# Kernel optimization log

Hardware: AMD Instinct MI355X
Metric: run time of the kernel (lower is better)

Reference implementation:

```python
import jax, jax.numpy as jnp
import numpy as np

E = 23   # unique_experts_num
K = 3    # act_experts_num
D = 1024 # in_features
H = 768  # hidden_features (0.75 * dim, per MOEBlock mlp_ratio)


def setup_inputs() -> dict:
    key = jax.random.key(0)
    ks = jax.random.split(key, 12)
    s_in = 1.0 / np.sqrt(D)
    s_hid = 1.0 / np.sqrt(H)
    x = jax.random.normal(ks[0], (4, 1024, D), dtype=jnp.float32)
    gate_W = jax.random.normal(ks[1], (D, E), dtype=jnp.float32) * s_in
    gate_b = jnp.zeros((E,), jnp.float32)
    bias = jnp.zeros((E,), jnp.float32)  # registered buffer, init to zeros
    W1 = jax.random.normal(ks[2], (E, D, H), dtype=jnp.float32) * s_in
    b1 = jnp.zeros((E, H), jnp.float32)
    W2 = jax.random.normal(ks[3], (E, H, D), dtype=jnp.float32) * s_hid
    b2 = jnp.zeros((E, D), jnp.float32)
    sW1 = jax.random.normal(ks[4], (D, H), dtype=jnp.float32) * s_in
    sb1 = jnp.zeros((H,), jnp.float32)
    sW2 = jax.random.normal(ks[5], (H, D), dtype=jnp.float32) * s_hid
    sb2 = jnp.zeros((D,), jnp.float32)
    return {"x": x, "gate_W": gate_W, "gate_b": gate_b, "bias": bias,
            "W1": W1, "b1": b1, "W2": W2, "b2": b2,
            "sW1": sW1, "sb1": sb1, "sW2": sW2, "sb2": sb2}


def reference(x, gate_W, gate_b, bias, W1, b1, W2, b2, sW1, sb1, sW2, sb2):
    o_shape = x.shape
    xt = x.reshape(-1, o_shape[-1])          # [T, D]
    T = xt.shape[0]

    # gating: sigmoid gate, top-k indices chosen on (gate + bias), weights gathered from gate
    gate = jax.nn.sigmoid(xt @ gate_W + gate_b)            # [T, E]
    _, top_idx = jax.lax.top_k(gate + bias, K)             # [T, K]
    top_w = jnp.take_along_axis(gate, top_idx, axis=-1)    # [T, K]
    top_w = top_w / jnp.sum(top_w, axis=-1, keepdims=True)

    # combine matrix: C[t, e] = normalized gate weight if e in top-k of token t else 0
    C = jnp.zeros((T, E), xt.dtype).at[jnp.arange(T)[:, None], top_idx].set(top_w)

    # all-expert dense compute (math-equivalent to dispatch/compute/combine)
    h = jax.nn.gelu(jnp.einsum('td,edh->eth', xt, W1) + b1[:, None, :], approximate=False)
    y = jnp.einsum('eth,ehd->etd', h, W2) + b2[:, None, :]  # [E, T, D]
    moe_out = jnp.einsum('etd,te->td', y, C)                # weighted combine

    # shared expert applied to every token
    shared = jax.nn.gelu(xt @ sW1 + sb1, approximate=False) @ sW2 + sb2
    out = shared + moe_out

    # aux load-balance loss
    gate_norm = gate / jnp.sum(gate, axis=-1, keepdims=True)
    P = jnp.mean(gate_norm, axis=0)                          # [E]
    counts = jnp.sum(jax.nn.one_hot(top_idx, E, dtype=jnp.float32), axis=(0, 1))  # [E]
    F = E * counts / (K * T)
    aux_loss = jnp.sum(P * F)

    return out.reshape(o_shape), aux_loss, counts.astype(jnp.int32)
```

## Files before the change

### kernel.cpp

```cpp
#include <hip/hip_runtime.h>
#include <math.h>

#define TT 4096
#define DD 1024
#define HH 768
#define NE 23
#define NG 24
#define BM 128
#define BN 128
#define BK 64
#define MAXT 160
#define KB1 16
#define KB2 12
#define NY1 6
#define NY2 8
#define NWG1 (MAXT*NY1)
#define NWG2 (MAXT*NY2)
#define GATE_BLKS 1024
#define CVT1_BLKS 2304
#define CVT_TOT   4608

#define WS_CURS   0
#define WS_OFFS   576
#define WS_TOTAL  640
#define WS_T2E    672
#define WS_T2A    832
#define WS_TOKE   1024
#define WS_TOKW   13312
#define WS_LTOK   25600
#define WS_LW     41984
#define WS_PPART  58368
#define WS_CPART  81920
#define WS_SIDX   106496
#define XB_OFF  ((size_t)524288)
#define H_OFF   ((size_t)8912896)
#define W1B_OFF ((size_t)34078720)
#define W2B_OFF ((size_t)71827456)

typedef short bf16x8 __attribute__((ext_vector_type(8)));
typedef float f32x4 __attribute__((ext_vector_type(4)));

#define S_BARRIER() asm volatile("s_barrier" ::: "memory")
#define WAIT_VM0()  asm volatile("s_waitcnt vmcnt(0)" ::: "memory")

__device__ inline unsigned short bfr(float f) {
    unsigned u = __float_as_uint(f);
    u += 0x7fffu + ((u >> 16) & 1u);
    return (unsigned short)(u >> 16);
}
__device__ inline unsigned bfr2(float lo, float hi) {
    return (unsigned)bfr(lo) | ((unsigned)bfr(hi) << 16);
}
__device__ inline float b2f(unsigned short u) {
    return __uint_as_float((unsigned)u << 16);
}

__device__ __forceinline__ void gl_lds16(const void* g, void* l) {
    __builtin_amdgcn_global_load_lds(
        (const __attribute__((address_space(1))) unsigned int*)g,
        (__attribute__((address_space(3))) unsigned int*)l, 16, 0, 0);
}

__global__ __launch_bounds__(256) void k_gatecvt(
    const float* __restrict__ x, const float* __restrict__ gW,
    const float* __restrict__ gb, const float* __restrict__ bias,
    const float* __restrict__ W1, const float* __restrict__ sW1,
    const float* __restrict__ W2, const float* __restrict__ sW2,
    int* __restrict__ tokE, float* __restrict__ tokW,
    float* __restrict__ Ppart, int* __restrict__ Cpart,
    unsigned short* __restrict__ xb,
    unsigned short* __restrict__ W1b, unsigned short* __restrict__ W2b)
{
    __shared__ __align__(16) char smem[16896];
    const int tid = threadIdx.x;

    if (blockIdx.x >= GATE_BLKS) {
        int id = blockIdx.x - GATE_BLKS;
        const float* src; unsigned short* dst;
        int N, kb0, n0, KBt, e;
        if (id < CVT1_BLKS) {
            N = HH; KBt = KB1;
            n0 = (id % 12) * 64; kb0 = ((id / 12) % 8) * 2; e = id / 96;
            src = (e < NE) ? (W1 + (size_t)e * DD * HH) : sW1;
            dst = W1b;
        } else {
            id -= CVT1_BLKS;
            N = DD; KBt = KB2;
            n0 = (id % 16) * 64; kb0 = ((id / 16) % 6) * 2; e = id / 96;
            src = (e < NE) ? (W2 + (size_t)e * HH * DD) : sW2;
            dst = W2b;
        }
        unsigned (*Ls)[32][65] = (unsigned (*)[32][65])smem;
        const int c = (tid & 15) * 4, r2l = tid >> 4;
        #pragma unroll
        for (int t = 0; t < 2; t++) {
            const float* tsrc = src + (size_t)(kb0 + t) * 64 * N + n0;
            #pragma unroll
            for (int pass = 0; pass < 2; pass++) {
                int row2 = pass * 16 + r2l;
                float4 v0 = *(const float4*)(tsrc + (size_t)(2 * row2) * N + c);
                float4 v1 = *(const float4*)(tsrc + (size_t)(2 * row2 + 1) * N + c);
                uint4 o;
                o.x = bfr2(v0.x, v1.x); o.y = bfr2(v0.y, v1.y);
                o.z = bfr2(v0.z, v1.z); o.w = bfr2(v0.w, v1.w);
                *(uint4*)&Ls[t][row2][c] = o;
            }
        }
        __syncthreads();
        #pragma unroll
        for (int t = 0; t < 2; t++) {
            unsigned short* dbase = dst + ((size_t)(e * KBt + kb0 + t) * N + n0) * 64;
            #pragma unroll
            for (int half = 0; half < 2; half++) {
                int g = half * 256 + tid;
                int n = g >> 3, p = g & 7;
                int j4 = (p ^ (n & 7)) * 4;
                uint4 o;
                o.x = Ls[t][j4 + 0][n]; o.y = Ls[t][j4 + 1][n];
                o.z = Ls[t][j4 + 2][n]; o.w = Ls[t][j4 + 3][n];
                *(uint4*)(dbase + n * 64 + p * 8) = o;
            }
        }
        return;
    }

    float (*xs)[DD] = (float (*)[DD])smem;
    float (*gv)[NE] = (float (*)[NE])(smem + 16384);
    float* ginvs    = (float*)(smem + 16768);
    int (*sel)[3]   = (int (*)[3])(smem + 16784);
    const int bid = blockIdx.x;
    const int t0 = bid * 4;
    {
        const float4* srcx = (const float4*)(x + (size_t)t0 * DD);
        float4* dstx = (float4*)&xs[0][0];
        #pragma unroll
        for (int i = 0; i < 4; i++) dstx[tid + 256 * i] = srcx[tid + 256 * i];
    }
    __syncthreads();
    {
        const float* xf = &xs[0][0];
        unsigned short* xd = xb + (size_t)t0 * DD;
        #pragma unroll
        for (int it = 0; it < 4; it++) {
            int o = it * 1024 + tid * 4;
            ushort4 u = make_ushort4(bfr(xf[o]), bfr(xf[o + 1]), bfr(xf[o + 2]), bfr(xf[o + 3]));
            *(ushort4*)(xd + o) = u;
        }
    }
    const int w = tid >> 6, l = tid & 63;
    const int t = t0 + w;
    if (l < NE) {
        const float* gc = gW + l;
        const float* xw = xs[w];
        float s[4] = {0.f, 0.f, 0.f, 0.f};
        #pragma unroll 2
        for (int d0 = 0; d0 < DD; d0 += 16) {
            float g[16];
            #pragma unroll
            for (int j = 0; j < 16; j++) g[j] = gc[(d0 + j) * NE];
            #pragma unroll
            for (int j = 0; j < 16; j++) s[j & 3] = fmaf(xw[d0 + j], g[j], s[j & 3]);
        }
        float sv = (s[0] + s[1]) + (s[2] + s[3]) + gb[l];
        gv[w][l] = 1.f / (1.f + expf(-sv));
    }
    __syncthreads();
    if (l == 0) {
        unsigned chosen = 0;
        int be[3]; float bw[3];
        float gsum = 0.f;
        for (int e = 0; e < NE; e++) gsum += gv[w][e];
        #pragma unroll
        for (int k = 0; k < 3; k++) {
            float m = -1e30f; int mi = 0;
            for (int e = 0; e < NE; e++) {
                float kv = gv[w][e] + bias[e];
                if (!((chosen >> e) & 1u) && kv > m) { m = kv; mi = e; }
            }
            chosen |= 1u << mi;
            be[k] = mi; bw[k] = gv[w][mi];
        }
        float inv = 1.f / (bw[0] + bw[1] + bw[2]);
        #pragma unroll
        for (int k = 0; k < 3; k++) {
            tokE[t * 3 + k] = be[k];
            tokW[t * 3 + k] = bw[k] * inv;
            sel[w][k] = be[k];
        }
        ginvs[w] = 1.f / gsum;
    }
    __syncthreads();
    if (tid < NE) {
        float p = gv[0][tid] * ginvs[0] + gv[1][tid] * ginvs[1]
                + gv[2][tid] * ginvs[2] + gv[3][tid] * ginvs[3];
        Ppart[tid * 1024 + bid] = p;
        int c = 0;
        #pragma unroll
        for (int w2 = 0; w2 < 4; w2++)
            #pragma unroll
            for (int k = 0; k < 3; k++) c += (sel[w2][k] == tid);
        Cpart[tid * 1024 + bid] = c;
    }
}

__global__ __launch_bounds__(256) void k_reduce(
    const float* __restrict__ Ppart, const int* __restrict__ Cpart,
    int* __restrict__ counts, float* __restrict__ Psum)
{
    const int e = blockIdx.x;
    const int tid = threadIdx.x;
    float s = 0.f; int c = 0;
    for (int i = tid; i < 1024; i += 256) {
        s += Ppart[e * 1024 + i];
        c += Cpart[e * 1024 + i];
    }
    #pragma unroll
    for (int off = 32; off >= 1; off >>= 1) {
        s += __shfl_down(s, off, 64);
        c += __shfl_down(c, off, 64);
    }
    __shared__ float ss[4]; __shared__ int sc[4];
    if ((tid & 63) == 0) { ss[tid >> 6] = s; sc[tid >> 6] = c; }
    __syncthreads();
    if (tid == 0) {
        Psum[e] = ss[0] + ss[1] + ss[2] + ss[3];
        counts[e] = sc[0] + sc[1] + sc[2] + sc[3];
    }
}

__global__ void k_scan(const int* __restrict__ counts, const float* __restrict__ Psum,
                       int* __restrict__ offs, int* __restrict__ total,
                       int* __restrict__ t2e, int* __restrict__ t2a,
                       int* __restrict__ curs, float* __restrict__ outAux)
{
    const int tid = threadIdx.x;
    for (int i = tid; i < NE * 16; i += 256) curs[i] = 0;
    if (tid != 0) return;
    int off = 0, toff = 0;
    for (int e = 0; e < NG; e++) {
        int c = (e < NE) ? counts[e] : TT;
        offs[e] = off;
        int nt = (c + BM - 1) / BM;
        for (int t = 0; t < nt; t++) {
            t2e[toff + t] = e;
            t2a[toff + t] = off + t * BM;
        }
        off += c; toff += nt;
    }
    offs[NG] = off;
    *total = toff;
    float aux = 0.f;
    for (int e = 0; e < NE; e++) {
        float P = Psum[e] / (float)TT;
        float F = (float)NE * (float)counts[e] / (float)(3 * TT);
        aux += P * F;
    }
    outAux[0] = aux;
    for (int e = 0; e < NE; e++) outAux[1 + e] = (float)counts[e];
}

__global__ void k_scatter(const int* __restrict__ tokE, const float* __restrict__ tokW,
                          const int* __restrict__ offs, int* __restrict__ curs,
                          int* __restrict__ ltok, float* __restrict__ lw,
                          int* __restrict__ sidx)
{
    int t = blockIdx.x * 256 + threadIdx.x;
    if (t >= TT) return;
    #pragma unroll
    for (int k = 0; k < 3; k++) {
        int e = tokE[t * 3 + k];
        int pos = atomicAdd(&curs[e * 16], 1);
        int idx = offs[e] + pos;
        ltok[idx] = t; lw[idx] = tokW[t * 3 + k];
        sidx[t * 3 + k] = idx;
    }
    ltok[3 * TT + t] = t;
    lw[3 * TT + t] = 1.f;
}

__global__ __launch_bounds__(256) void k_mm1(
    const unsigned short* __restrict__ xb, const unsigned short* __restrict__ W1b,
    const float* __restrict__ b1, const float* __restrict__ sb1,
    const int* __restrict__ t2e, const int* __restrict__ t2a,
    const int* __restrict__ offs, const int* __restrict__ total,
    const int* __restrict__ ltok, unsigned short* __restrict__ H)
{
    const int id = blockIdx.x;
    const int wg = (id & 7) * (NWG1 / 8) + (id >> 3);
    const int ns = wg / MAXT;
    const int tb = wg % MAXT;
    if (tb >= *total) return;
    const int e = t2e[tb];
    const int a0 = t2a[tb];
    const int acount = min(offs[e + 1] - a0, BM);
    const float* bb = (e < NE) ? (b1 + e * HH) : sb1;
    const int nb = ns * BN;

    __shared__ unsigned short As[2][BM * BK];
    __shared__ unsigned short Bs[2][BN * BK];
    __shared__ int rows[BM];
    const int tid = threadIdx.x;
    if (tid < BM) rows[tid] = ltok[a0 + min(tid, acount - 1)];
    __syncthreads();

    const int wid = tid >> 6, lane = tid & 63;
    const int wr = wid >> 1, wc = wid & 1;
    const int l15 = lane & 15, l4 = lane >> 4;

    float bv[4];
    #pragma unroll
    for (int n = 0; n < 4; n++) bv[n] = bb[nb + wc * 64 + n * 16 + l15];

    f32x4 acc[4][4];
    #pragma unroll
    for (int m = 0; m < 4; m++)
        #pragma unroll
        for (int n = 0; n < 4; n++) acc[m][n] = (f32x4){0.f, 0.f, 0.f, 0.f};

    const unsigned short* aSrc[4];
    int Goff[4];
    #pragma unroll
    for (int c = 0; c < 4; c++) {
        int G = (wid * 4 + c) * 64 + lane;
        int row = G >> 3, j = G & 7;
        aSrc[c] = xb + (size_t)rows[row] * DD + ((j ^ (row & 7)) << 3);
        Goff[c] = G * 8;
    }
    const unsigned short* wbase = W1b + ((size_t)e * KB1 * HH + nb) * 64;

    auto stage = [&](int buf, int kb) {
        #pragma unroll
        for (int c = 0; c < 4; c++)
            gl_lds16(aSrc[c] + kb * 64, &As[buf][Goff[c]]);
        const unsigned short* wb = wbase + (size_t)kb * (HH * 64);
        #pragma unroll
        for (int c = 0; c < 4; c++)
            gl_lds16(wb + Goff[c], &Bs[buf][Goff[c]]);
    };
    auto compute = [&](int buf) {
        #pragma unroll
        for (int kh = 0; kh < 2; kh++) {
            bf16x8 af[4], bf[4];
            #pragma unroll
            for (int f = 0; f < 4; f++) {
                int ar = wr * 64 + f * 16 + l15;
                int br = wc * 64 + f * 16 + l15;
                int pg = (kh << 2) + l4;
                af[f] = *(const bf16x8*)&As[buf][ar * 64 + ((pg ^ (ar & 7)) << 3)];
                bf[f] = *(const bf16x8*)&Bs[buf][br * 64 + ((pg ^ (br & 7)) << 3)];
            }
            #pragma unroll
            for (int m = 0; m < 4; m++)
                #pragma unroll
                for (int n = 0; n < 4; n++)
                    acc[m][n] = __builtin_amdgcn_mfma_f32_16x16x32_bf16(af[m], bf[n], acc[m][n], 0, 0, 0);
        }
    };

    stage(0, 0);
    WAIT_VM0();
    S_BARRIER();
    int cur = 0;
    #pragma unroll 1
    for (int kb = 0; kb < KB1; kb++) {
        if (kb + 1 < KB1) stage(cur ^ 1, kb + 1);
        __builtin_amdgcn_sched_barrier(0);
        compute(cur);
        if (kb + 1 < KB1) {
            WAIT_VM0();
            S_BARRIER();
            cur ^= 1;
        }
    }

    #pragma unroll
    for (int m = 0; m < 4; m++) {
        int rbase = wr * 64 + m * 16 + l4 * 4;
        #pragma unroll
        for (int n = 0; n < 4; n++) {
            int col = nb + wc * 64 + n * 16 + l15;
            #pragma unroll
            for (int i = 0; i < 4; i++) {
                int r = rbase + i;
                if (r < acount) {
                    float v = acc[m][n][i] + bv[n];
                    float u = v + 0.044715f * v * v * v;
                    float g = v / (1.f + __expf(-1.5957691216f * u));
                    H[(size_t)(a0 + r) * HH + col] = bfr(g);
                }
            }
        }
    }
}

__global__ __launch_bounds__(256) void k_mm2(
    const unsigned short* __restrict__ H, const unsigned short* __restrict__ W2b,
    const float* __restrict__ b2, const float* __restrict__ sb2,
    const int* __restrict__ t2e, const int* __restrict__ t2a,
    const int* __restrict__ offs, const int* __restrict__ total,
    const int* __restrict__ ltok, const float* __restrict__ lw,
    unsigned short* __restrict__ yslot, float* __restrict__ out)
{
    const int id = blockIdx.x;
    const int wg = (id & 7) * (NWG2 / 8) + (id >> 3);
    const int ns = wg / MAXT;
    const int tb = wg % MAXT;
    if (tb >= *total) return;
    const int e = t2e[tb];
    const int a0 = t2a[tb];
    const int acount = min(offs[e + 1] - a0, BM);
    const float* bb = (e < NE) ? (b2 + e * DD) : sb2;
    const int nb = ns * BN;

    __shared__ unsigned short As[2][BM * BK];
    __shared__ unsigned short Bs[2][BN * BK];
    __shared__ int rows[BM];
    __shared__ float wts[BM];
    const int tid = threadIdx.x;
    if (tid < BM) {
        rows[tid] = (tid < acount) ? ltok[a0 + tid] : -1;
        wts[tid]  = (tid < acount) ? lw[a0 + tid] : 0.f;
    }
    __syncthreads();

    const int wid = tid >> 6, lane = tid & 63;
    const int wr = wid >> 1, wc = wid & 1;
    const int l15 = lane & 15, l4 = lane >> 4;

    float bv[4];
    #pragma unroll
    for (int n = 0; n < 4; n++) bv[n] = bb[nb + wc * 64 + n * 16 + l15];

    f32x4 acc[4][4];
    #pragma unroll
    for (int m = 0; m < 4; m++)
        #pragma unroll
        for (int n = 0; n < 4; n++) acc[m][n] = (f32x4){0.f, 0.f, 0.f, 0.f};

    const unsigned short* aSrc[4];
    int Goff[4];
    #pragma unroll
    for (int c = 0; c < 4; c++) {
        int G = (wid * 4 + c) * 64 + lane;
        int row = G >> 3, j = G & 7;
        aSrc[c] = H + (size_t)(a0 + row) * HH + ((j ^ (row & 7)) << 3);
        Goff[c] = G * 8;
    }
    const unsigned short* wbase = W2b + ((size_t)e * KB2 * DD + nb) * 64;

    auto stage = [&](int buf, int kb) {
        #pragma unroll
        for (int c = 0; c < 4; c++)
            gl_lds16(aSrc[c] + kb * 64, &As[buf][Goff[c]]);
        const unsigned short* wb = wbase + (size_t)kb * (DD * 64);
        #pragma unroll
        for (int c = 0; c < 4; c++)
            gl_lds16(wb + Goff[c], &Bs[buf][Goff[c]]);
    };
    auto compute = [&](int buf) {
        #pragma unroll
        for (int kh = 0; kh < 2; kh++) {
            bf16x8 af[4], bf[4];
            #pragma unroll
            for (int f = 0; f < 4; f++) {
                int ar = wr * 64 + f * 16 + l15;
                int br = wc * 64 + f * 16 + l15;
                int pg = (kh << 2) + l4;
                af[f] = *(const bf16x8*)&As[buf][ar * 64 + ((pg ^ (ar & 7)) << 3)];
                bf[f] = *(const bf16x8*)&Bs[buf][br * 64 + ((pg ^ (br & 7)) << 3)];
            }
            #pragma unroll
            for (int m = 0; m < 4; m++)
                #pragma unroll
                for (int n = 0; n < 4; n++)
                    acc[m][n] = __builtin_amdgcn_mfma_f32_16x16x32_bf16(af[m], bf[n], acc[m][n], 0, 0, 0);
        }
    };

    stage(0, 0);
    WAIT_VM0();
    S_BARRIER();
    int cur = 0;
    #pragma unroll 1
    for (int kb = 0; kb < KB2; kb++) {
        if (kb + 1 < KB2) stage(cur ^ 1, kb + 1);
        __builtin_amdgcn_sched_barrier(0);
        compute(cur);
        if (kb + 1 < KB2) {
            WAIT_VM0();
            S_BARRIER();
            cur ^= 1;
        }
    }

    if (e == NE) {
        #pragma unroll
        for (int m = 0; m < 4; m++) {
            int rbase = wr * 64 + m * 16 + l4 * 4;
            #pragma unroll
            for (int n = 0; n < 4; n++) {
                int col = nb + wc * 64 + n * 16 + l15;
                #pragma unroll
                for (int i = 0; i < 4; i++) {
                    int r = rbase + i;
                    out[(size_t)rows[r] * DD + col] = acc[m][n][i] + bv[n];
                }
            }
        }
    } else {
        #pragma unroll
        for (int m = 0; m < 4; m++) {
            int rbase = wr * 64 + m * 16 + l4 * 4;
            #pragma unroll
            for (int n = 0; n < 4; n++) {
                int col = nb + wc * 64 + n * 16 + l15;
                #pragma unroll
                for (int i = 0; i < 4; i++) {
                    int r = rbase + i;
                    if (r < acount)
                        yslot[(size_t)(a0 + r) * DD + col] = bfr(wts[r] * (acc[m][n][i] + bv[n]));
                }
            }
        }
    }
}

__global__ __launch_bounds__(256) void k_combine(
    const unsigned short* __restrict__ yslot, const int* __restrict__ sidx,
    float* __restrict__ out)
{
    const int t = blockIdx.x;
    const int s0 = sidx[t * 3 + 0], s1 = sidx[t * 3 + 1], s2 = sidx[t * 3 + 2];
    const int d = threadIdx.x * 4;
    float* o = out + (size_t)t * DD + d;
    float4 v = *(float4*)o;
    ushort4 a = *(const ushort4*)(yslot + (size_t)s0 * DD + d);
    ushort4 b = *(const ushort4*)(yslot + (size_t)s1 * DD + d);
    ushort4 c = *(const ushort4*)(yslot + (size_t)s2 * DD + d);
    v.x += b2f(a.x) + b2f(b.x) + b2f(c.x);
    v.y += b2f(a.y) + b2f(b.y) + b2f(c.y);
    v.z += b2f(a.z) + b2f(b.z) + b2f(c.z);
    v.w += b2f(a.w) + b2f(b.w) + b2f(c.w);
    *(float4*)o = v;
}

extern "C" void kernel_launch(void* const* d_in, const int* in_sizes, int n_in,
                              void* d_out, int out_size, void* d_ws, size_t ws_size,
                              hipStream_t stream)
{
    const float* x    = (const float*)d_in[0];
    const float* gW   = (const float*)d_in[1];
    const float* gb   = (const float*)d_in[2];
    const float* bias = (const float*)d_in[3];
    const float* W1   = (const float*)d_in[4];
    const float* b1   = (const float*)d_in[5];
    const float* W2   = (const float*)d_in[6];
    const float* b2   = (const float*)d_in[7];
    const float* sW1  = (const float*)d_in[8];
    const float* sb1  = (const float*)d_in[9];
    const float* sW2  = (const float*)d_in[10];
    const float* sb2  = (const float*)d_in[11];
    float* out = (float*)d_out;
    float* wsf = (float*)d_ws;
    int*   wsi = (int*)d_ws;

    int*   curs   = wsi + WS_CURS;
    int*   offs   = wsi + WS_OFFS;
    int*   total  = wsi + WS_TOTAL;
    int*   t2e    = wsi + WS_T2E;
    int*   t2a    = wsi + WS_T2A;
    int*   tokE   = wsi + WS_TOKE;
    float* tokW   = wsf + WS_TOKW;
    int*   ltok   = wsi + WS_LTOK;
    float* lwt    = wsf + WS_LW;
    float* Ppart  = wsf + WS_PPART;
    int*   Cpart  = wsi + WS_CPART;
    int*   sidx   = wsi + WS_SIDX;
    int*   counts = wsi + 432;
    float* Psum   = wsf + 464;
    unsigned short* xb  = (unsigned short*)((char*)d_ws + XB_OFF);
    unsigned short* Hb  = (unsigned short*)((char*)d_ws + H_OFF);
    unsigned short* W1b = (unsigned short*)((char*)d_ws + W1B_OFF);
    unsigned short* W2b = (unsigned short*)((char*)d_ws + W2B_OFF);
    unsigned short* yslot = W1b;

    k_gatecvt<<<GATE_BLKS + CVT_TOT, 256, 0, stream>>>(
        x, gW, gb, bias, W1, sW1, W2, sW2, tokE, tokW, Ppart, Cpart, xb, W1b, W2b);
    k_reduce<<<NE, 256, 0, stream>>>(Ppart, Cpart, counts, Psum);
    k_scan<<<1, 256, 0, stream>>>(counts, Psum, offs, total, t2e, t2a, curs,
                                  out + (size_t)TT * DD);
    k_scatter<<<TT / 256, 256, 0, stream>>>(tokE, tokW, offs, curs, ltok, lwt, sidx);
    k_mm1<<<NWG1, 256, 0, stream>>>(xb, W1b, b1, sb1, t2e, t2a, offs, total, ltok, Hb);
    k_mm2<<<NWG2, 256, 0, stream>>>(Hb, W2b, b2, sb2, t2e, t2a, offs, total, ltok, lwt,
                                    yslot, out);
    k_combine<<<TT, 256, 0, stream>>>(yslot, sidx, out);
}
```

Baseline: 213.0 us.

## Move W2 bf16 conversion into mm1 launch to overlap with GEMM

The fp32-to-bf16 conversion of W2/sW2 moves out of the first gating kernel and into extra blocks appended to the mm1 GEMM launch. The first kernel only converts W1, so its critical path shrinks, and the W2 conversion can fill CUs left idle by early-exiting mm1 tiles. In exchange mm1 now uses dynamic-sized shared arrays carved from one buffer, and the conversion blocks compete with the GEMM for bandwidth and CU slots.

Result: slower. 221.9 us (+4.2%).

```diff
diff --git a/kernel.cpp b/kernel.cpp
--- a/kernel.cpp
+++ b/kernel.cpp
@@ -18,7 +18,7 @@
 #define NWG2 (MAXT*NY2)
 #define GATE_BLKS 1024
 #define CVT1_BLKS 2304
-#define CVT_TOT   4608
+#define CVT2_BLKS 2304
 
 #define WS_CURS   0
 #define WS_OFFS   576
@@ -61,66 +61,59 @@
         (__attribute__((address_space(3))) unsigned int*)l, 16, 0, 0);
 }
 
-__global__ __launch_bounds__(256) void k_gatecvt(
+__device__ __forceinline__ void cvt_tile(
+    const float* __restrict__ src, unsigned short* __restrict__ dst,
+    int N, int KBt, int e, int kb0, int n0, void* smem, int tid)
+{
+    unsigned (*Ls)[32][65] = (unsigned (*)[32][65])smem;
+    const int c = (tid & 15) * 4, r2l = tid >> 4;
+    #pragma unroll
+    for (int t = 0; t < 2; t++) {
+        const float* tsrc = src + (size_t)(kb0 + t) * 64 * N + n0;
+        #pragma unroll
+        for (int pass = 0; pass < 2; pass++) {
+            int row2 = pass * 16 + r2l;
+            float4 v0 = *(const float4*)(tsrc + (size_t)(2 * row2) * N + c);
+            float4 v1 = *(const float4*)(tsrc + (size_t)(2 * row2 + 1) * N + c);
+            uint4 o;
+            o.x = bfr2(v0.x, v1.x); o.y = bfr2(v0.y, v1.y);
+            o.z = bfr2(v0.z, v1.z); o.w = bfr2(v0.w, v1.w);
+            *(uint4*)&Ls[t][row2][c] = o;
+        }
+    }
+    __syncthreads();
+    #pragma unroll
+    for (int t = 0; t < 2; t++) {
+        unsigned short* dbase = dst + ((size_t)(e * KBt + kb0 + t) * N + n0) * 64;
+        #pragma unroll
+        for (int half = 0; half < 2; half++) {
+            int g = half * 256 + tid;
+            int n = g >> 3, p = g & 7;
+            int j4 = (p ^ (n & 7)) * 4;
+            uint4 o;
+            o.x = Ls[t][j4 + 0][n]; o.y = Ls[t][j4 + 1][n];
+            o.z = Ls[t][j4 + 2][n]; o.w = Ls[t][j4 + 3][n];
+            *(uint4*)(dbase + n * 64 + p * 8) = o;
+        }
+    }
+}
+
+__global__ __launch_bounds__(256) void k_gatecvt1(
     const float* __restrict__ x, const float* __restrict__ gW,
     const float* __restrict__ gb, const float* __restrict__ bias,
     const float* __restrict__ W1, const float* __restrict__ sW1,
-    const float* __restrict__ W2, const float* __restrict__ sW2,
     int* __restrict__ tokE, float* __restrict__ tokW,
     float* __restrict__ Ppart, int* __restrict__ Cpart,
-    unsigned short* __restrict__ xb,
-    unsigned short* __restrict__ W1b, unsigned short* __restrict__ W2b)
+    unsigned short* __restrict__ xb, unsigned short* __restrict__ W1b)
 {
     __shared__ __align__(16) char smem[16896];
     const int tid = threadIdx.x;
 
     if (blockIdx.x >= GATE_BLKS) {
         int id = blockIdx.x - GATE_BLKS;
-        const float* src; unsigned short* dst;
-        int N, kb0, n0, KBt, e;
-        if (id < CVT1_BLKS) {
-            N = HH; KBt = KB1;
-            n0 = (id % 12) * 64; kb0 = ((id / 12) % 8) * 2; e = id / 96;
-            src = (e < NE) ? (W1 + (size_t)e * DD * HH) : sW1;
-            dst = W1b;
-        } else {
-            id -= CVT1_BLKS;
-            N = DD; KBt = KB2;
-            n0 = (id % 16) * 64; kb0 = ((id / 16) % 6) * 2; e = id / 96;
-            src = (e < NE) ? (W2 + (size_t)e * HH * DD) : sW2;
-            dst = W2b;
-        }
-        unsigned (*Ls)[32][65] = (unsigned (*)[32][65])smem;
-        const int c = (tid & 15) * 4, r2l = tid >> 4;
-        #pragma unroll
-        for (int t = 0; t < 2; t++) {
-            const float* tsrc = src + (size_t)(kb0 + t) * 64 * N + n0;
-            #pragma unroll
-            for (int pass = 0; pass < 2; pass++) {
-                int row2 = pass * 16 + r2l;
-                float4 v0 = *(const float4*)(tsrc + (size_t)(2 * row2) * N + c);
-                float4 v1 = *(const float4*)(tsrc + (size_t)(2 * row2 + 1) * N + c);
-                uint4 o;
-                o.x = bfr2(v0.x, v1.x); o.y = bfr2(v0.y, v1.y);
-                o.z = bfr2(v0.z, v1.z); o.w = bfr2(v0.w, v1.w);
-                *(uint4*)&Ls[t][row2][c] = o;
-            }
-        }
-        __syncthreads();
-        #pragma unroll
-        for (int t = 0; t < 2; t++) {
-            unsigned short* dbase = dst + ((size_t)(e * KBt + kb0 + t) * N + n0) * 64;
-            #pragma unroll
-            for (int half = 0; half < 2; half++) {
-                int g = half * 256 + tid;
-                int n = g >> 3, p = g & 7;
-                int j4 = (p ^ (n & 7)) * 4;
-                uint4 o;
-                o.x = Ls[t][j4 + 0][n]; o.y = Ls[t][j4 + 1][n];
-                o.z = Ls[t][j4 + 2][n]; o.w = Ls[t][j4 + 3][n];
-                *(uint4*)(dbase + n * 64 + p * 8) = o;
-            }
-        }
+        int n0 = (id % 12) * 64, kb0 = ((id / 12) % 8) * 2, e = id / 96;
+        const float* src = (e < NE) ? (W1 + (size_t)e * DD * HH) : sW1;
+        cvt_tile(src, W1b, HH, KB1, e, kb0, n0, smem, tid);
         return;
     }
 
@@ -278,13 +271,30 @@
     lw[3 * TT + t] = 1.f;
 }
 
-__global__ __launch_bounds__(256) void k_mm1(
+__global__ __launch_bounds__(256) void k_mm1cvt(
     const unsigned short* __restrict__ xb, const unsigned short* __restrict__ W1b,
     const float* __restrict__ b1, const float* __restrict__ sb1,
+    const float* __restrict__ W2, const float* __restrict__ sW2,
     const int* __restrict__ t2e, const int* __restrict__ t2a,
     const int* __restrict__ offs, const int* __restrict__ total,
-    const int* __restrict__ ltok, unsigned short* __restrict__ H)
-{
+    const int* __restrict__ ltok, unsigned short* __restrict__ H,
+    unsigned short* __restrict__ W2b)
+{
+    __shared__ __align__(16) char smem[66048];
+    const int tid = threadIdx.x;
+
+    if (blockIdx.x >= NWG1) {
+        int id = blockIdx.x - NWG1;
+        int n0 = (id % 16) * 64, kb0 = ((id / 16) % 6) * 2, e = id / 96;
+        const float* src = (e < NE) ? (W2 + (size_t)e * HH * DD) : sW2;
+        cvt_tile(src, W2b, DD, KB2, e, kb0, n0, smem, tid);
+        return;
+    }
+
+    unsigned short (*As)[BM * BK] = (unsigned short (*)[BM * BK])smem;
+    unsigned short (*Bs)[BN * BK] = (unsigned short (*)[BN * BK])(smem + 32768);
+    int* rows = (int*)(smem + 65536);
+
     const int id = blockIdx.x;
     const int wg = (id & 7) * (NWG1 / 8) + (id >> 3);
     const int ns = wg / MAXT;
@@ -296,10 +306,6 @@
     const float* bb = (e < NE) ? (b1 + e * HH) : sb1;
     const int nb = ns * BN;
 
-    __shared__ unsigned short As[2][BM * BK];
-    __shared__ unsigned short Bs[2][BN * BK];
-    __shared__ int rows[BM];
-    const int tid = threadIdx.x;
     if (tid < BM) rows[tid] = ltok[a0 + min(tid, acount - 1)];
     __syncthreads();
 
@@ -584,13 +590,14 @@
     unsigned short* W2b = (unsigned short*)((char*)d_ws + W2B_OFF);
     unsigned short* yslot = W1b;
 
-    k_gatecvt<<<GATE_BLKS + CVT_TOT, 256, 0, stream>>>(
-        x, gW, gb, bias, W1, sW1, W2, sW2, tokE, tokW, Ppart, Cpart, xb, W1b, W2b);
+    k_gatecvt1<<<GATE_BLKS + CVT1_BLKS, 256, 0, stream>>>(
+        x, gW, gb, bias, W1, sW1, tokE, tokW, Ppart, Cpart, xb, W1b);
     k_reduce<<<NE, 256, 0, stream>>>(Ppart, Cpart, counts, Psum);
     k_scan<<<1, 256, 0, stream>>>(counts, Psum, offs, total, t2e, t2a, curs,
                                   out + (size_t)TT * DD);
     k_scatter<<<TT / 256, 256, 0, stream>>>(tokE, tokW, offs, curs, ltok, lwt, sidx);
-    k_mm1<<<NWG1, 256, 0, stream>>>(xb, W1b, b1, sb1, t2e, t2a, offs, total, ltok, Hb);
+    k_mm1cvt<<<NWG1 + CVT2_BLKS, 256, 0, stream>>>(
+        xb, W1b, b1, sb1, W2, sW2, t2e, t2a, offs, total, ltok, Hb, W2b);
     k_mm2<<<NWG2, 256, 0, stream>>>(Hb, W2b, b2, sb2, t2e, t2a, offs, total, ltok, lwt,
                                     yslot, out);
     k_combine<<<TT, 256, 0, stream>>>(yslot, sidx, out);
```

## Enlarge grouped GEMM tiles to 256x256 with 512-thread blocks

Applied to the files above, without the earlier changes.

Doubles the M and N tile sizes of both expert GEMM kernels to 256x256, runs them with 8 waves per block, and gives each wave a 64x128 output sub-tile with 32 accumulators. Fewer row tiles and column splits are launched, so each staged weight and activation tile is reused across more output, cutting global and LDS traffic per FLOP. In exchange, padding waste per expert grows because of the coarser row tiles, register pressure and LDS use per block rise, occupancy falls, and fewer blocks may underfill the GPU. The weight conversion code is also moved into a helper function with no change in behaviour.

Result: slower. 246.5 us (+15.7%).

```diff
diff --git a/kernel.cpp b/kernel.cpp
--- a/kernel.cpp
+++ b/kernel.cpp
@@ -6,14 +6,14 @@
 #define HH 768
 #define NE 23
 #define NG 24
-#define BM 128
-#define BN 128
+#define BM 256
+#define BN 256
 #define BK 64
-#define MAXT 160
+#define MAXT 88
 #define KB1 16
 #define KB2 12
-#define NY1 6
-#define NY2 8
+#define NY1 3
+#define NY2 4
 #define NWG1 (MAXT*NY1)
 #define NWG2 (MAXT*NY2)
 #define GATE_BLKS 1024
@@ -61,6 +61,43 @@
         (__attribute__((address_space(3))) unsigned int*)l, 16, 0, 0);
 }
 
+__device__ __forceinline__ void cvt_tile(
+    const float* __restrict__ src, unsigned short* __restrict__ dst,
+    int N, int KBt, int e, int kb0, int n0, void* smem, int tid)
+{
+    unsigned (*Ls)[32][65] = (unsigned (*)[32][65])smem;
+    const int c = (tid & 15) * 4, r2l = tid >> 4;
+    #pragma unroll
+    for (int t = 0; t < 2; t++) {
+        const float* tsrc = src + (size_t)(kb0 + t) * 64 * N + n0;
+        #pragma unroll
+        for (int pass = 0; pass < 2; pass++) {
+            int row2 = pass * 16 + r2l;
+            float4 v0 = *(const float4*)(tsrc + (size_t)(2 * row2) * N + c);
+            float4 v1 = *(const float4*)(tsrc + (size_t)(2 * row2 + 1) * N + c);
+            uint4 o;
+            o.x = bfr2(v0.x, v1.x); o.y = bfr2(v0.y, v1.y);
+            o.z = bfr2(v0.z, v1.z); o.w = bfr2(v0.w, v1.w);
+            *(uint4*)&Ls[t][row2][c] = o;
+        }
+    }
+    __syncthreads();
+    #pragma unroll
+    for (int t = 0; t < 2; t++) {
+        unsigned short* dbase = dst + ((size_t)(e * KBt + kb0 + t) * N + n0) * 64;
+        #pragma unroll
+        for (int half = 0; half < 2; half++) {
+            int g = half * 256 + tid;
+            int n = g >> 3, p = g & 7;
+            int j4 = (p ^ (n & 7)) * 4;
+            uint4 o;
+            o.x = Ls[t][j4 + 0][n]; o.y = Ls[t][j4 + 1][n];
+            o.z = Ls[t][j4 + 2][n]; o.w = Ls[t][j4 + 3][n];
+            *(uint4*)(dbase + n * 64 + p * 8) = o;
+        }
+    }
+}
+
 __global__ __launch_bounds__(256) void k_gatecvt(
     const float* __restrict__ x, const float* __restrict__ gW,
     const float* __restrict__ gb, const float* __restrict__ bias,
@@ -76,50 +113,15 @@
 
     if (blockIdx.x >= GATE_BLKS) {
         int id = blockIdx.x - GATE_BLKS;
-        const float* src; unsigned short* dst;
-        int N, kb0, n0, KBt, e;
         if (id < CVT1_BLKS) {
-            N = HH; KBt = KB1;
-            n0 = (id % 12) * 64; kb0 = ((id / 12) % 8) * 2; e = id / 96;
-            src = (e < NE) ? (W1 + (size_t)e * DD * HH) : sW1;
-            dst = W1b;
+            int n0 = (id % 12) * 64, kb0 = ((id / 12) % 8) * 2, e = id / 96;
+            const float* src = (e < NE) ? (W1 + (size_t)e * DD * HH) : sW1;
+            cvt_tile(src, W1b, HH, KB1, e, kb0, n0, smem, tid);
         } else {
             id -= CVT1_BLKS;
-            N = DD; KBt = KB2;
-            n0 = (id % 16) * 64; kb0 = ((id / 16) % 6) * 2; e = id / 96;
-            src = (e < NE) ? (W2 + (size_t)e * HH * DD) : sW2;
-            dst = W2b;
-        }
-        unsigned (*Ls)[32][65] = (unsigned (*)[32][65])smem;
-        const int c = (tid & 15) * 4, r2l = tid >> 4;
-        #pragma unroll
-        for (int t = 0; t < 2; t++) {
-            const float* tsrc = src + (size_t)(kb0 + t) * 64 * N + n0;
-            #pragma unroll
-            for (int pass = 0; pass < 2; pass++) {
-                int row2 = pass * 16 + r2l;
-                float4 v0 = *(const float4*)(tsrc + (size_t)(2 * row2) * N + c);
-                float4 v1 = *(const float4*)(tsrc + (size_t)(2 * row2 + 1) * N + c);
-                uint4 o;
-                o.x = bfr2(v0.x, v1.x); o.y = bfr2(v0.y, v1.y);
-                o.z = bfr2(v0.z, v1.z); o.w = bfr2(v0.w, v1.w);
-                *(uint4*)&Ls[t][row2][c] = o;
-            }
-        }
-        __syncthreads();
-        #pragma unroll
-        for (int t = 0; t < 2; t++) {
-            unsigned short* dbase = dst + ((size_t)(e * KBt + kb0 + t) * N + n0) * 64;
-            #pragma unroll
-            for (int half = 0; half < 2; half++) {
-                int g = half * 256 + tid;
-                int n = g >> 3, p = g & 7;
-                int j4 = (p ^ (n & 7)) * 4;
-                uint4 o;
-                o.x = Ls[t][j4 + 0][n]; o.y = Ls[t][j4 + 1][n];
-                o.z = Ls[t][j4 + 2][n]; o.w = Ls[t][j4 + 3][n];
-                *(uint4*)(dbase + n * 64 + p * 8) = o;
-            }
+            int n0 = (id % 16) * 64, kb0 = ((id / 16) % 6) * 2, e = id / 96;
+            const float* src = (e < NE) ? (W2 + (size_t)e * HH * DD) : sW2;
+            cvt_tile(src, W2b, DD, KB2, e, kb0, n0, smem, tid);
         }
         return;
     }
@@ -278,7 +280,7 @@
     lw[3 * TT + t] = 1.f;
 }
 
-__global__ __launch_bounds__(256) void k_mm1(
+__global__ __launch_bounds__(512) void k_mm1(
     const unsigned short* __restrict__ xb, const unsigned short* __restrict__ W1b,
     const float* __restrict__ b1, const float* __restrict__ sb1,
     const int* __restrict__ t2e, const int* __restrict__ t2a,
@@ -304,55 +306,59 @@
     __syncthreads();
 
     const int wid = tid >> 6, lane = tid & 63;
-    const int wr = wid >> 1, wc = wid & 1;
+    const int wr = wid & 3, wc = wid >> 2;
     const int l15 = lane & 15, l4 = lane >> 4;
 
-    float bv[4];
-    #pragma unroll
-    for (int n = 0; n < 4; n++) bv[n] = bb[nb + wc * 64 + n * 16 + l15];
-
-    f32x4 acc[4][4];
+    float bv[8];
+    #pragma unroll
+    for (int n = 0; n < 8; n++) bv[n] = bb[nb + wc * 128 + n * 16 + l15];
+
+    f32x4 acc[4][8];
     #pragma unroll
     for (int m = 0; m < 4; m++)
         #pragma unroll
-        for (int n = 0; n < 4; n++) acc[m][n] = (f32x4){0.f, 0.f, 0.f, 0.f};
+        for (int n = 0; n < 8; n++) acc[m][n] = (f32x4){0.f, 0.f, 0.f, 0.f};
 
     const unsigned short* aSrc[4];
-    int Goff[4];
+    int GA[4];
     #pragma unroll
     for (int c = 0; c < 4; c++) {
-        int G = (wid * 4 + c) * 64 + lane;
+        int G = c * 512 + tid;
         int row = G >> 3, j = G & 7;
         aSrc[c] = xb + (size_t)rows[row] * DD + ((j ^ (row & 7)) << 3);
-        Goff[c] = G * 8;
+        GA[c] = G * 8;
     }
     const unsigned short* wbase = W1b + ((size_t)e * KB1 * HH + nb) * 64;
 
     auto stage = [&](int buf, int kb) {
         #pragma unroll
         for (int c = 0; c < 4; c++)
-            gl_lds16(aSrc[c] + kb * 64, &As[buf][Goff[c]]);
+            gl_lds16(aSrc[c] + kb * 64, &As[buf][GA[c]]);
         const unsigned short* wb = wbase + (size_t)kb * (HH * 64);
         #pragma unroll
         for (int c = 0; c < 4; c++)
-            gl_lds16(wb + Goff[c], &Bs[buf][Goff[c]]);
+            gl_lds16(wb + GA[c], &Bs[buf][GA[c]]);
     };
     auto compute = [&](int buf) {
         #pragma unroll
         for (int kh = 0; kh < 2; kh++) {
-            bf16x8 af[4], bf[4];
+            bf16x8 af[4], bf[8];
             #pragma unroll
             for (int f = 0; f < 4; f++) {
                 int ar = wr * 64 + f * 16 + l15;
-                int br = wc * 64 + f * 16 + l15;
                 int pg = (kh << 2) + l4;
                 af[f] = *(const bf16x8*)&As[buf][ar * 64 + ((pg ^ (ar & 7)) << 3)];
+            }
+            #pragma unroll
+            for (int f = 0; f < 8; f++) {
+                int br = wc * 128 + f * 16 + l15;
+                int pg = (kh << 2) + l4;
                 bf[f] = *(const bf16x8*)&Bs[buf][br * 64 + ((pg ^ (br & 7)) << 3)];
             }
             #pragma unroll
             for (int m = 0; m < 4; m++)
                 #pragma unroll
-                for (int n = 0; n < 4; n++)
+                for (int n = 0; n < 8; n++)
                     acc[m][n] = __builtin_amdgcn_mfma_f32_16x16x32_bf16(af[m], bf[n], acc[m][n], 0, 0, 0);
         }
     };
@@ -377,8 +383,8 @@
     for (int m = 0; m < 4; m++) {
         int rbase = wr * 64 + m * 16 + l4 * 4;
         #pragma unroll
-        for (int n = 0; n < 4; n++) {
-            int col = nb + wc * 64 + n * 16 + l15;
+        for (int n = 0; n < 8; n++) {
+            int col = nb + wc * 128 + n * 16 + l15;
             #pragma unroll
             for (int i = 0; i < 4; i++) {
                 int r = rbase + i;
@@ -393,7 +399,7 @@
     }
 }
 
-__global__ __launch_bounds__(256) void k_mm2(
+__global__ __launch_bounds__(512) void k_mm2(
     const unsigned short* __restrict__ H, const unsigned short* __restrict__ W2b,
     const float* __restrict__ b2, const float* __restrict__ sb2,
     const int* __restrict__ t2e, const int* __restrict__ t2a,
@@ -424,55 +430,59 @@
     __syncthreads();
 
     const int wid = tid >> 6, lane = tid & 63;
-    const int wr = wid >> 1, wc = wid & 1;
+    const int wr = wid & 3, wc = wid >> 2;
     const int l15 = lane & 15, l4 = lane >> 4;
 
-    float bv[4];
-    #pragma unroll
-    for (int n = 0; n < 4; n++) bv[n] = bb[nb + wc * 64 + n * 16 + l15];
-
-    f32x4 acc[4][4];
+    float bv[8];
+    #pragma unroll
+    for (int n = 0; n < 8; n++) bv[n] = bb[nb + wc * 128 + n * 16 + l15];
+
+    f32x4 acc[4][8];
     #pragma unroll
     for (int m = 0; m < 4; m++)
         #pragma unroll
-        for (int n = 0; n < 4; n++) acc[m][n] = (f32x4){0.f, 0.f, 0.f, 0.f};
+        for (int n = 0; n < 8; n++) acc[m][n] = (f32x4){0.f, 0.f, 0.f, 0.f};
 
     const unsigned short* aSrc[4];
-    int Goff[4];
+    int GA[4];
     #pragma unroll
     for (int c = 0; c < 4; c++) {
-        int G = (wid * 4 + c) * 64 + lane;
+        int G = c * 512 + tid;
         int row = G >> 3, j = G & 7;
         aSrc[c] = H + (size_t)(a0 + row) * HH + ((j ^ (row & 7)) << 3);
-        Goff[c] = G * 8;
+        GA[c] = G * 8;
     }
     const unsigned short* wbase = W2b + ((size_t)e * KB2 * DD + nb) * 64;
 
     auto stage = [&](int buf, int kb) {
         #pragma unroll
         for (int c = 0; c < 4; c++)
-            gl_lds16(aSrc[c] + kb * 64, &As[buf][Goff[c]]);
+            gl_lds16(aSrc[c] + kb * 64, &As[buf][GA[c]]);
         const unsigned short* wb = wbase + (size_t)kb * (DD * 64);
         #pragma unroll
         for (int c = 0; c < 4; c++)
-            gl_lds16(wb + Goff[c], &Bs[buf][Goff[c]]);
+            gl_lds16(wb + GA[c], &Bs[buf][GA[c]]);
     };
     auto compute = [&](int buf) {
         #pragma unroll
         for (int kh = 0; kh < 2; kh++) {
-            bf16x8 af[4], bf[4];
+            bf16x8 af[4], bf[8];
             #pragma unroll
             for (int f = 0; f < 4; f++) {
                 int ar = wr * 64 + f * 16 + l15;
-                int br = wc * 64 + f * 16 + l15;
                 int pg = (kh << 2) + l4;
                 af[f] = *(const bf16x8*)&As[buf][ar * 64 + ((pg ^ (ar & 7)) << 3)];
+            }
+            #pragma unroll
+            for (int f = 0; f < 8; f++) {
+                int br = wc * 128 + f * 16 + l15;
+                int pg = (kh << 2) + l4;
                 bf[f] = *(const bf16x8*)&Bs[buf][br * 64 + ((pg ^ (br & 7)) << 3)];
             }
             #pragma unroll
             for (int m = 0; m < 4; m++)
                 #pragma unroll
-                for (int n = 0; n < 4; n++)
+                for (int n = 0; n < 8; n++)
                     acc[m][n] = __builtin_amdgcn_mfma_f32_16x16x32_bf16(af[m], bf[n], acc[m][n], 0, 0, 0);
         }
     };
@@ -498,8 +508,8 @@
         for (int m = 0; m < 4; m++) {
             int rbase = wr * 64 + m * 16 + l4 * 4;
             #pragma unroll
-            for (int n = 0; n < 4; n++) {
-                int col = nb + wc * 64 + n * 16 + l15;
+            for (int n = 0; n < 8; n++) {
+                int col = nb + wc * 128 + n * 16 + l15;
                 #pragma unroll
                 for (int i = 0; i < 4; i++) {
                     int r = rbase + i;
@@ -512,8 +522,8 @@
         for (int m = 0; m < 4; m++) {
             int rbase = wr * 64 + m * 16 + l4 * 4;
             #pragma unroll
-            for (int n = 0; n < 4; n++) {
-                int col = nb + wc * 64 + n * 16 + l15;
+            for (int n = 0; n < 8; n++) {
+                int col = nb + wc * 128 + n * 16 + l15;
                 #pragma unroll
                 for (int i = 0; i < 4; i++) {
                     int r = rbase + i;
@@ -590,8 +600,8 @@
     k_scan<<<1, 256, 0, stream>>>(counts, Psum, offs, total, t2e, t2a, curs,
                                   out + (size_t)TT * DD);
     k_scatter<<<TT / 256, 256, 0, stream>>>(tokE, tokW, offs, curs, ltok, lwt, sidx);
-    k_mm1<<<NWG1, 256, 0, stream>>>(xb, W1b, b1, sb1, t2e, t2a, offs, total, ltok, Hb);
-    k_mm2<<<NWG2, 256, 0, stream>>>(Hb, W2b, b2, sb2, t2e, t2a, offs, total, ltok, lwt,
+    k_mm1<<<NWG1, 512, 0, stream>>>(xb, W1b, b1, sb1, t2e, t2a, offs, total, ltok, Hb);
+    k_mm2<<<NWG2, 512, 0, stream>>>(Hb, W2b, b2, sb2, t2e, t2a, offs, total, ltok, lwt,
                                     yslot, out);
     k_combine<<<TT, 256, 0, stream>>>(yslot, sidx, out);
 }
```
